# Kernel optimization log

Measured on AMD Instinct MI355X. Metric: run time of the kernel, lower is better.

The kernel has to match this reference:

```python
import jax, jax.numpy as jnp
import numpy as np

N_USERS = 100000
N_ITEMS = 50000
DIM = 64
HID = 64
E = 3200000
B = 16384


def setup_inputs() -> dict:
    key = jax.random.key(0)
    ks = jax.random.split(key, 16)
    N = N_USERS + N_ITEMS
    return {
        "users": jax.random.randint(ks[0], (B,), 0, N_USERS),
        "items": jax.random.randint(ks[1], (B,), 0, N_ITEMS),
        "edge_index": jax.random.randint(ks[2], (2, E), 0, N),
        "edge_weight": jax.random.uniform(ks[3], (E,), dtype=jnp.float32),
        # learned parameters
        "U": jax.random.normal(ks[4], (N_USERS, DIM), jnp.float32) * 0.1,
        "I": jax.random.normal(ks[5], (N_ITEMS, DIM), jnp.float32) * 0.1,
        "W0": jax.random.normal(ks[6], (DIM, HID), jnp.float32) / np.sqrt(DIM),
        "b0": jnp.zeros((HID,), jnp.float32),
        "g0": jnp.ones((HID,), jnp.float32),
        "be0": jnp.zeros((HID,), jnp.float32),
        "W1": jax.random.normal(ks[7], (HID, HID), jnp.float32) / np.sqrt(HID),
        "b1": jnp.zeros((HID,), jnp.float32),
        "g1": jnp.ones((HID,), jnp.float32),
        "be1": jnp.zeros((HID,), jnp.float32),
        "Wp": jax.random.normal(ks[8], (HID, DIM), jnp.float32) / np.sqrt(HID),
        "bp": jnp.zeros((DIM,), jnp.float32),
        "bu": jnp.zeros((N_USERS,), jnp.float32),
        "bi": jnp.zeros((N_ITEMS,), jnp.float32),
        "mu": jnp.zeros((), jnp.float32),
    }


def _layernorm(h, g, b, eps=1e-5):
    m = jnp.mean(h, axis=-1, keepdims=True)
    v = jnp.mean(jnp.square(h - m), axis=-1, keepdims=True)
    return (h - m) * jax.lax.rsqrt(v + eps) * g + b


def reference(users, items, edge_index, edge_weight, U, I,
              W0, b0, g0, be0, W1, b1, g1, be1, Wp, bp, bu, bi, mu):
    N = U.shape[0] + I.shape[0]
    x = jnp.concatenate([U, I], axis=0)  # [N, DIM]

    # GCN normalization with added self-loops (torch_geometric gcn_norm)
    loop = jnp.arange(N)
    src = jnp.concatenate([edge_index[0], loop])
    dst = jnp.concatenate([edge_index[1], loop])
    ew = jnp.concatenate([edge_weight, jnp.ones((N,), edge_weight.dtype)])
    deg = jax.ops.segment_sum(ew, dst, num_segments=N)
    dinv = jnp.where(deg > 0, jax.lax.rsqrt(deg), 0.0)
    norm = dinv[src] * ew * dinv[dst]  # [E+N]

    def conv(h, W, b):
        hw = h @ W  # [N, HID]
        msgs = norm[:, None] * hw[src]  # gather: [E+N, HID]
        return jax.ops.segment_sum(msgs, dst, num_segments=N) + b

    # layer 0: conv -> layernorm -> relu -> (dropout=identity, eval) -> residual
    h = x
    h_in = h
    h = conv(h, W0, b0)
    h = jax.nn.relu(_layernorm(h, g0, be0)) + h_in
    # layer 1
    h_in = h
    h = conv(h, W1, b1)
    h = jax.nn.relu(_layernorm(h, g1, be1)) + h_in

    h = h @ Wp + bp  # proj_out: [N, DIM]
    h_user = h[:U.shape[0]]
    h_item = h[U.shape[0]:]

    s = jnp.sum(h_user[users] * h_item[items], axis=-1)
    s = s + bu[users] + bi[items] + mu
    return jnp.clip(s, 1.0, 5.0)
```

## Files before the change

### kernel.cpp

```cpp
#include <hip/hip_runtime.h>

#define NU 100000
#define NI 50000
#define NN 150000
#define D  64
#define CAP 47
#define OVF_MAX 4096

#define BINSHIFT 8
#define BINW 256
#define NBINS 586
#define BINCAP 5848
#define STAGE_CAP 11
#define EPT 4
#define SPILL_CAP 262144
#define BIN_BLOCKS 768
#define BCPAD 16

typedef unsigned int uint;
typedef unsigned short ushort;
typedef unsigned char uchar;

__device__ __forceinline__ float half_reduce_add(float v) {
    #pragma unroll
    for (int m = 16; m >= 1; m >>= 1) v += __shfl_xor(v, m, 64);
    return v;
}
__device__ __forceinline__ ushort f2bf(float f) {
    union { float f; uint i; } c; c.f = f;
    uint r = c.i + 0x7FFF + ((c.i >> 16) & 1);
    return (ushort)(r >> 16);
}
__device__ __forceinline__ float lane_bcast(float v, int l) {
    return __int_as_float(__builtin_amdgcn_readlane(__float_as_int(v), l));
}
__device__ __forceinline__ uint enc14(float w) {
    uint b = __float_as_uint(w) + 0x00020000u;
    return b & 0xFFFC0000u;
}
__device__ __forceinline__ float dec14(uint r) {
    return __uint_as_float(r & 0xFFFC0000u);
}
__device__ __forceinline__ void spill_one(int d, uint s, float w,
        uint2* __restrict__ spill, int* __restrict__ spillcnt) {
    int si = atomicAdd(spillcnt, 1);
    if (si < SPILL_CAP) spill[si] = make_uint2(s | enc14(w), (uint)d);
}

__global__ __launch_bounds__(256) void k_bin(
        const int* __restrict__ src, const int* __restrict__ dst,
        const float* __restrict__ ew, int* __restrict__ bincur,
        uint2* __restrict__ binbuf, uint2* __restrict__ spill,
        int* __restrict__ spillcnt, uint2* __restrict__ tail,
        uchar* __restrict__ cnt8, int E) {
    __shared__ uint2 stage[NBINS][STAGE_CAP];
    __shared__ int scnt[NBINS];
    int t = threadIdx.x;
    for (int i = t; i < NBINS; i += 256) scnt[i] = 0;
    __syncthreads();
    const int batch = 256 * EPT;
    for (int base = blockIdx.x * batch; base < E; base += BIN_BLOCKS * batch) {
        int dd[EPT]; uint ss[EPT]; float ww[EPT]; int ok[EPT];
        #pragma unroll
        for (int k = 0; k < EPT; ++k) {
            int e = base + k * 256 + t;
            ok[k] = (e < E);
            if (ok[k]) { dd[k] = dst[e]; ss[k] = (uint)src[e]; ww[k] = ew[e]; }
        }
        #pragma unroll
        for (int k = 0; k < EPT; ++k) {
            if (!ok[k]) continue;
            int bin = dd[k] >> BINSHIFT;
            int slot = atomicAdd(&scnt[bin], 1);
            if (slot < STAGE_CAP) {
                stage[bin][slot] = make_uint2(
                    ss[k] | ((uint)(dd[k] & (BINW - 1)) << 18),
                    (uint)__float_as_int(ww[k]));
            } else {
                spill_one(dd[k], ss[k], ww[k], spill, spillcnt);
            }
        }
        __syncthreads();
        for (int bin = t; bin < NBINS; bin += 256) {
            int c = scnt[bin]; if (c > STAGE_CAP) c = STAGE_CAP;
            while (c >= 8) {
                int b0 = atomicAdd(&bincur[bin * BCPAD], 8);
                if (b0 + 8 <= BINCAP) {
                    uint4* o4 = (uint4*)(binbuf + (size_t)bin * BINCAP + b0);
                    uint2* s2 = &stage[bin][c - 8];
                    o4[0] = make_uint4(s2[0].x, s2[0].y, s2[1].x, s2[1].y);
                    o4[1] = make_uint4(s2[2].x, s2[2].y, s2[3].x, s2[3].y);
                    o4[2] = make_uint4(s2[4].x, s2[4].y, s2[5].x, s2[5].y);
                    o4[3] = make_uint4(s2[6].x, s2[6].y, s2[7].x, s2[7].y);
                } else {
                    for (int j = 0; j < 8; ++j) {
                        uint2 r = stage[bin][c - 8 + j];
                        spill_one((bin << BINSHIFT) + (int)(r.x >> 18),
                                  r.x & 0x3FFFFu, __int_as_float((int)r.y),
                                  spill, spillcnt);
                    }
                }
                c -= 8;
            }
            scnt[bin] = c;
        }
        __syncthreads();
    }
    uchar* cb = cnt8 + (size_t)blockIdx.x * NBINS;
    for (int i = t; i < NBINS; i += 256) cb[i] = (uchar)scnt[i];
    uint2* tb = tail + (size_t)blockIdx.x * (NBINS * 8);
    for (int i = t; i < NBINS * 8; i += 256) tb[i] = stage[i >> 3][i & 7];
}

__global__ __launch_bounds__(256) void k_regroup(
        const int* __restrict__ bincur, const uint2* __restrict__ binbuf,
        const uint2* __restrict__ spill, const int* __restrict__ spillcnt,
        const uint2* __restrict__ tail, const uchar* __restrict__ cnt8,
        uint* __restrict__ recs, int* __restrict__ cursor,
        float* __restrict__ dinv, int4* __restrict__ ovf,
        int* __restrict__ ovfcnt) {
    __shared__ uint image[256 * CAP];
    __shared__ int cnt[256];
    __shared__ float ovfw[256];
    int t = threadIdx.x;
    int bin = blockIdx.x;
    cnt[t] = 0; ovfw[t] = 0.0f;
    __syncthreads();
    int dbase = bin << BINSHIFT;
    int nrec = bincur[bin * BCPAD]; if (nrec > BINCAP) nrec = BINCAP;
    const uint2* bb = binbuf + (size_t)bin * BINCAP;
    for (int i = t; i < nrec; i += 256) {
        uint2 r = bb[i];
        int dl = (int)(r.x >> 18);
        int slot = atomicAdd(&cnt[dl], 1);
        uint s = r.x & 0x3FFFFu;
        float w = __int_as_float((int)r.y);
        if (slot < CAP) image[dl * CAP + slot] = enc14(w) | s;
        else {
            atomicAdd(&ovfw[dl], w);
            int o = atomicAdd(ovfcnt, 1);
            if (o < OVF_MAX)
                ovf[o] = make_int4(dbase + dl, (int)s, __float_as_int(w), 0);
        }
    }
    for (int g = t; g < BIN_BLOCKS; g += 256) {
        int c = cnt8[(size_t)g * NBINS + bin];
        const uint2* tb = tail + ((size_t)g * NBINS + bin) * 8;
        for (int j = 0; j < c; ++j) {
            uint2 r = tb[j];
            int dl = (int)(r.x >> 18);
            int slot = atomicAdd(&cnt[dl], 1);
            uint s = r.x & 0x3FFFFu;
            float w = __int_as_float((int)r.y);
            if (slot < CAP) image[dl * CAP + slot] = enc14(w) | s;
            else {
                atomicAdd(&ovfw[dl], w);
                int o = atomicAdd(ovfcnt, 1);
                if (o < OVF_MAX)
                    ovf[o] = make_int4(dbase + dl, (int)s, __float_as_int(w), 0);
            }
        }
    }
    int ns = spillcnt[0]; if (ns > SPILL_CAP) ns = SPILL_CAP;
    for (int i = t; i < ns; i += 256) {
        uint2 e = spill[i];
        int d = (int)e.y;
        if (d < dbase || d >= dbase + BINW) continue;
        int dl = d - dbase;
        int slot = atomicAdd(&cnt[dl], 1);
        if (slot < CAP) image[dl * CAP + slot] = e.x;
        else {
            float w = dec14(e.x);
            atomicAdd(&ovfw[dl], w);
            int o = atomicAdd(ovfcnt, 1);
            if (o < OVF_MAX) ovf[o] = make_int4(d, (int)(e.x & 0x3FFFFu),
                                                __float_as_int(w), 0);
        }
    }
    __syncthreads();
    int ndl = NN - dbase; if (ndl > 256) ndl = 256;
    if (ndl <= 0) return;
    if (t < ndl) {
        int c = cnt[t];
        cursor[dbase + t] = c;
        if (c > CAP) c = CAP;
        float dg = ovfw[t];
        for (int j = 0; j < c; ++j) dg += dec14(image[t * CAP + j]);
        dinv[dbase + t] = rsqrtf(dg + 1.0f);
    }
    int tot = ndl * CAP;
    uint* out = recs + (size_t)dbase * CAP;
    for (int i = t; i < tot; i += 256) out[i] = image[i];
}

__global__ __launch_bounds__(256) void k_gemm1(
        const float* __restrict__ U, const float* __restrict__ I,
        const float* __restrict__ W, const float* __restrict__ dinv,
        ushort* __restrict__ out) {
    int lane = threadIdx.x & 63;
    float wreg[64];
    #pragma unroll
    for (int k = 0; k < 64; ++k) wreg[k] = W[k * 64 + lane];
    int wpb = blockDim.x >> 6;
    int wid = blockIdx.x * wpb + (threadIdx.x >> 6);
    int tw = gridDim.x * wpb;
    for (int n = wid; n < NN; n += tw) {
        float xv = (n < NU) ? U[(size_t)n * D + lane]
                            : I[(size_t)(n - NU) * D + lane];
        float a0 = 0.f, a1 = 0.f, a2 = 0.f, a3 = 0.f;
        #pragma unroll
        for (int k = 0; k < 64; k += 4) {
            a0 = fmaf(lane_bcast(xv, k + 0), wreg[k + 0], a0);
            a1 = fmaf(lane_bcast(xv, k + 1), wreg[k + 1], a1);
            a2 = fmaf(lane_bcast(xv, k + 2), wreg[k + 2], a2);
            a3 = fmaf(lane_bcast(xv, k + 3), wreg[k + 3], a3);
        }
        out[(size_t)n * D + lane] = f2bf(((a0 + a1) + (a2 + a3)) * dinv[n]);
    }
}

#define CA_DECL(c) uint x##c##0, x##c##1, x##c##2, x##c##3, \
                        w##c##0, w##c##1, w##c##2, w##c##3;
#define CA_GET(c, i, P, rvv) { \
    uint r = (uint)__builtin_amdgcn_ds_bpermute(vodd4 + 8 * (P), (int)(rvv)); \
    w##c##i = r & 0xFFFC0000u; \
    x##c##i = *(const uint*)((const char*)hw2p + \
                             (((r & 0x3FFFFu) << 7) + lb4)); }
#define CA_ISSUE(c, P0, rvv) { CA_GET(c, 0, (P0)+0, rvv) CA_GET(c, 1, (P0)+1, rvv) \
                               CA_GET(c, 2, (P0)+2, rvv) CA_GET(c, 3, (P0)+3, rvv) }
#define CA_FMA1(c, i, axv, ayv) { \
    axv = fmaf(__uint_as_float(w##c##i), __uint_as_float(x##c##i << 16), axv); \
    ayv = fmaf(__uint_as_float(w##c##i), \
               __uint_as_float(x##c##i & 0xFFFF0000u), ayv); }
#define CA_FMA(c, axv, ayv) { CA_FMA1(c,0,axv,ayv) CA_FMA1(c,1,axv,ayv) \
                              CA_FMA1(c,2,axv,ayv) CA_FMA1(c,3,axv,ayv) }

__device__ __forceinline__ float2 conv_accum2(int n, int lane,
        const uint* __restrict__ hw2p, const int* __restrict__ cursor,
        const uint* __restrict__ recs, const int4* __restrict__ ovf,
        const int* __restrict__ ovfcnt) {
    int cnt = __builtin_amdgcn_readfirstlane(cursor[n]);
    if (cnt > CAP) cnt = CAP;
    uint rv = (lane < cnt) ? recs[(size_t)n * CAP + lane] : 0u;
    const int  vodd4 = (lane >> 5) << 2;
    const uint lb4   = (uint)(lane & 31) << 2;
    uint xs = *(const uint*)((const char*)hw2p + (((uint)n << 7) + lb4));
    float ax = 0.f, ay = 0.f;
    int cp = (cnt + 7) & ~7;
    CA_DECL(A) CA_DECL(B) CA_DECL(G)
    CA_ISSUE(A, 0, rv) CA_ISSUE(B, 4, rv) CA_ISSUE(G, 8, rv)
    CA_FMA(A, ax, ay)
    if (cp > 24) CA_ISSUE(A, 12, rv)
    CA_FMA(B, ax, ay)
    if (cp > 32) CA_ISSUE(B, 16, rv)
    CA_FMA(G, ax, ay)
    if (cp > 40) CA_ISSUE(G, 20, rv)
    if (cp > 24) CA_FMA(A, ax, ay)
    if (cp > 32) CA_FMA(B, ax, ay)
    if (cp > 40) CA_FMA(G, ax, ay)
    ax += __shfl_xor(ax, 32, 64);
    ay += __shfl_xor(ay, 32, 64);
    ax += __uint_as_float(xs << 16);
    ay += __uint_as_float(xs & 0xFFFF0000u);
    int novf = __builtin_amdgcn_readfirstlane(ovfcnt[0]);
    if (novf > 0) {
        if (novf > OVF_MAX) novf = OVF_MAX;
        for (int j = 0; j < novf; ++j) {
            int4 e = ovf[j];
            if (e.x == n) {
                float w = __int_as_float(e.z);
                uint x = hw2p[(size_t)e.y * 32 + (lane & 31)];
                ax = fmaf(w, __int_as_float((int)(x << 16)), ax);
                ay = fmaf(w, __int_as_float((int)(x & 0xFFFF0000u)), ay);
            }
        }
    }
    return make_float2(ax, ay);
}

__device__ __forceinline__ float2 ln_relu2(float2 a, float di, int p,
        const float* __restrict__ b, const float* __restrict__ g,
        const float* __restrict__ be) {
    float2 bb = ((const float2*)b)[p];
    float v0 = fmaf(a.x, di, bb.x);
    float v1 = fmaf(a.y, di, bb.y);
    float m = half_reduce_add(v0 + v1) * (1.0f / 64.0f);
    float d0 = v0 - m, d1 = v1 - m;
    float var = half_reduce_add(d0 * d0 + d1 * d1) * (1.0f / 64.0f);
    float rs = rsqrtf(var + 1e-5f);
    float2 gg = ((const float2*)g)[p];
    float2 ee = ((const float2*)be)[p];
    return make_float2(fmaxf(fmaf(d0 * rs, gg.x, ee.x), 0.0f),
                       fmaxf(fmaf(d1 * rs, gg.y, ee.y), 0.0f));
}

__global__ __launch_bounds__(256) void k_conv1(
        const uint* __restrict__ hw2p, const int* __restrict__ cursor,
        const uint* __restrict__ recs, const int4* __restrict__ ovf,
        const int* __restrict__ ovfcnt, const float* __restrict__ dinv,
        const float* __restrict__ b, const float* __restrict__ g,
        const float* __restrict__ be, const float* __restrict__ U,
        const float* __restrict__ I, uint* __restrict__ out1) {
    int lane = threadIdx.x & 63;
    int n = __builtin_amdgcn_readfirstlane(blockIdx.x * 4 + (threadIdx.x >> 6));
    if (n >= NN) return;
    float2 a = conv_accum2(n, lane, hw2p, cursor, recs, ovf, ovfcnt);
    int p = lane & 31;
    float2 y = ln_relu2(a, dinv[n], p, b, g, be);
    const float* R = (n < NU) ? (U + (size_t)n * D) : (I + (size_t)(n - NU) * D);
    float2 rr = ((const float2*)R)[p];
    if (lane < 32) {
        out1[(size_t)n * 32 + p] =
            (uint)f2bf(y.x + rr.x) | ((uint)f2bf(y.y + rr.y) << 16);
    }
}

#define CB_DECL(p, c) uint p##x##c##0, p##x##c##1, p##x##c##2, p##x##c##3, \
                           p##w##c##0, p##w##c##1, p##w##c##2, p##w##c##3;
#define CB_GET(p, c, i, P, rvv) { \
    uint r = (uint)__builtin_amdgcn_ds_bpermute(vodd4 + 8 * (P), (int)(rvv)); \
    p##w##c##i = r & 0xFFFC0000u; \
    p##x##c##i = *(const uint*)((const char*)hw2p + \
                                (((r & 0x3FFFFu) << 7) + lb4)); }
#define CB_ISSUE(p, c, P0, rvv) { CB_GET(p,c,0,(P0)+0,rvv) CB_GET(p,c,1,(P0)+1,rvv) \
                                  CB_GET(p,c,2,(P0)+2,rvv) CB_GET(p,c,3,(P0)+3,rvv) }
#define CB_FMA1(p, c, i, axv, ayv) { \
    axv = fmaf(__uint_as_float(p##w##c##i), \
               __uint_as_float(p##x##c##i << 16), axv); \
    ayv = fmaf(__uint_as_float(p##w##c##i), \
               __uint_as_float(p##x##c##i & 0xFFFF0000u), ayv); }
#define CB_FMA(p, c, axv, ayv) { CB_FMA1(p,c,0,axv,ayv) CB_FMA1(p,c,1,axv,ayv) \
                                 CB_FMA1(p,c,2,axv,ayv) CB_FMA1(p,c,3,axv,ayv) }

__device__ __forceinline__ void conv_accum2_dual(int nu, int ni, int lane,
        const uint* __restrict__ hw2p, const int* __restrict__ cursor,
        const uint* __restrict__ recs, const int4* __restrict__ ovf,
        const int* __restrict__ ovfcnt, float2* outu, float2* outi) {
    int cu = __builtin_amdgcn_readfirstlane(cursor[nu]); if (cu > CAP) cu = CAP;
    int ci = __builtin_amdgcn_readfirstlane(cursor[ni]); if (ci > CAP) ci = CAP;
    uint rvu = (lane < cu) ? recs[(size_t)nu * CAP + lane] : 0u;
    uint rvi = (lane < ci) ? recs[(size_t)ni * CAP + lane] : 0u;
    const int  vodd4 = (lane >> 5) << 2;
    const uint lb4   = (uint)(lane & 31) << 2;
    uint xsu = *(const uint*)((const char*)hw2p + (((uint)nu << 7) + lb4));
    uint xsi = *(const uint*)((const char*)hw2p + (((uint)ni << 7) + lb4));
    float uax = 0.f, uay = 0.f, iax = 0.f, iay = 0.f;
    int cpu_ = (cu + 7) & ~7, cpi_ = (ci + 7) & ~7;
    CB_DECL(u, A) CB_DECL(u, B) CB_DECL(u, G)
    CB_DECL(i, A) CB_DECL(i, B) CB_DECL(i, G)
    CB_ISSUE(u, A, 0, rvu) CB_ISSUE(i, A, 0, rvi)
    CB_ISSUE(u, B, 4, rvu) CB_ISSUE(i, B, 4, rvi)
    CB_ISSUE(u, G, 8, rvu) CB_ISSUE(i, G, 8, rvi)
    CB_FMA(u, A, uax, uay) CB_FMA(i, A, iax, iay)
    if (cpu_ > 24) CB_ISSUE(u, A, 12, rvu)
    if (cpi_ > 24) CB_ISSUE(i, A, 12, rvi)
    CB_FMA(u, B, uax, uay) CB_FMA(i, B, iax, iay)
    if (cpu_ > 32) CB_ISSUE(u, B, 16, rvu)
    if (cpi_ > 32) CB_ISSUE(i, B, 16, rvi)
    CB_FMA(u, G, uax, uay) CB_FMA(i, G, iax, iay)
    if (cpu_ > 40) CB_ISSUE(u, G, 20, rvu)
    if (cpi_ > 40) CB_ISSUE(i, G, 20, rvi)
    if (cpu_ > 24) CB_FMA(u, A, uax, uay)
    if (cpi_ > 24) CB_FMA(i, A, iax, iay)
    if (cpu_ > 32) CB_FMA(u, B, uax, uay)
    if (cpi_ > 32) CB_FMA(i, B, iax, iay)
    if (cpu_ > 40) CB_FMA(u, G, uax, uay)
    if (cpi_ > 40) CB_FMA(i, G, iax, iay)
    uax += __shfl_xor(uax, 32, 64); uay += __shfl_xor(uay, 32, 64);
    iax += __shfl_xor(iax, 32, 64); iay += __shfl_xor(iay, 32, 64);
    uax += __uint_as_float(xsu << 16); uay += __uint_as_float(xsu & 0xFFFF0000u);
    iax += __uint_as_float(xsi << 16); iay += __uint_as_float(xsi & 0xFFFF0000u);
    int novf = __builtin_amdgcn_readfirstlane(ovfcnt[0]);
    if (novf > 0) {
        if (novf > OVF_MAX) novf = OVF_MAX;
        for (int j = 0; j < novf; ++j) {
            int4 e = ovf[j];
            if (e.x == nu || e.x == ni) {
                float w = __int_as_float(e.z);
                uint x = hw2p[(size_t)e.y * 32 + (lane & 31)];
                float fx = __uint_as_float(x << 16);
                float fy = __uint_as_float(x & 0xFFFF0000u);
                if (e.x == nu) { uax = fmaf(w, fx, uax); uay = fmaf(w, fy, uay); }
                else           { iax = fmaf(w, fx, iax); iay = fmaf(w, fy, iay); }
            }
        }
    }
    *outu = make_float2(uax, uay);
    *outi = make_float2(iax, iay);
}

__global__ __launch_bounds__(256) void k_gemm2(
        const ushort* __restrict__ hb, const float* __restrict__ W,
        const float* __restrict__ dinv, ushort* __restrict__ out) {
    int lane = threadIdx.x & 63;
    float wreg[64];
    #pragma unroll
    for (int k = 0; k < 64; ++k) wreg[k] = W[k * 64 + lane];
    int wpb = blockDim.x >> 6;
    int wid = blockIdx.x * wpb + (threadIdx.x >> 6);
    int tw = gridDim.x * wpb;
    for (int n = wid; n < NN; n += tw) {
        float xv = __uint_as_float((uint)hb[(size_t)n * D + lane] << 16);
        float a0 = 0.f, a1 = 0.f, a2 = 0.f, a3 = 0.f;
        #pragma unroll
        for (int k = 0; k < 64; k += 4) {
            a0 = fmaf(lane_bcast(xv, k + 0), wreg[k + 0], a0);
            a1 = fmaf(lane_bcast(xv, k + 1), wreg[k + 1], a1);
            a2 = fmaf(lane_bcast(xv, k + 2), wreg[k + 2], a2);
            a3 = fmaf(lane_bcast(xv, k + 3), wreg[k + 3], a3);
        }
        out[(size_t)n * D + lane] = f2bf(((a0 + a1) + (a2 + a3)) * dinv[n]);
    }
}

__global__ __launch_bounds__(256) void k_conv2score(
        const uint* __restrict__ hw2p, const int* __restrict__ cursor,
        const uint* __restrict__ recs, const int4* __restrict__ ovf,
        const int* __restrict__ ovfcnt, const float* __restrict__ dinv,
        const float* __restrict__ b, const float* __restrict__ g,
        const float* __restrict__ be, const int* __restrict__ users,
        const int* __restrict__ items, const uint* __restrict__ h1b,
        const float* __restrict__ Wp, const float* __restrict__ bp,
        const float* __restrict__ bu, const float* __restrict__ bi,
        const float* __restrict__ mu, float* __restrict__ out, int B) {
    __shared__ float wlds[64 * 64];
    int t = threadIdx.x;
    for (int i = t; i < 64 * 64; i += 256) wlds[i] = Wp[i];
    __syncthreads();
    int lane = t & 63;
    float bpl = bp[lane];
    int q = lane & 31;
    int wpb = blockDim.x >> 6;
    int wid = blockIdx.x * wpb + (t >> 6);
    int tw = gridDim.x * wpb;
    for (int p = wid; p < B; p += tw) {
        int un = users[p];
        int in_ = NU + items[p];
        int nu = __builtin_amdgcn_readfirstlane(un);
        int ni = __builtin_amdgcn_readfirstlane(in_);
        float2 au, ai;
        conv_accum2_dual(nu, ni, lane, hw2p, cursor, recs, ovf, ovfcnt,
                         &au, &ai);
        float2 yu = ln_relu2(au, dinv[nu], q, b, g, be);
        float2 yi = ln_relu2(ai, dinv[ni], q, b, g, be);
        uint xu = h1b[(size_t)nu * 32 + q];
        uint xi = h1b[(size_t)ni * 32 + q];
        float2 hu = make_float2(yu.x + __uint_as_float(xu << 16),
                                yu.y + __uint_as_float(xu & 0xFFFF0000u));
        float2 hi = make_float2(yi.x + __uint_as_float(xi << 16),
                                yi.y + __uint_as_float(xi & 0xFFFF0000u));
        float pu = bpl, pi = bpl;
        #pragma unroll
        for (int j = 0; j < 32; ++j) {
            float w0 = wlds[(2 * j) * 64 + lane];
            float w1 = wlds[(2 * j + 1) * 64 + lane];
            pu = fmaf(lane_bcast(hu.x, j), w0, pu);
            pu = fmaf(lane_bcast(hu.y, j), w1, pu);
            pi = fmaf(lane_bcast(hi.x, j), w0, pi);
            pi = fmaf(lane_bcast(hi.y, j), w1, pi);
        }
        float dot = pu * pi;
        #pragma unroll
        for (int m = 32; m >= 1; m >>= 1) dot += __shfl_xor(dot, m, 64);
        if (lane == 0) {
            dot += bu[un] + bi[in_ - NU] + mu[0];
            out[p] = fminf(fmaxf(dot, 1.0f), 5.0f);
        }
    }
}

extern "C" void kernel_launch(void* const* d_in, const int* in_sizes, int n_in,
                              void* d_out, int out_size, void* d_ws, size_t ws_size,
                              hipStream_t stream) {
    const int*   users = (const int*)d_in[0];
    const int*   items = (const int*)d_in[1];
    const int*   ei2   = (const int*)d_in[2];
    const float* ew    = (const float*)d_in[3];
    const float* U     = (const float*)d_in[4];
    const float* I     = (const float*)d_in[5];
    const float* W0    = (const float*)d_in[6];
    const float* b0    = (const float*)d_in[7];
    const float* g0    = (const float*)d_in[8];
    const float* be0   = (const float*)d_in[9];
    const float* W1    = (const float*)d_in[10];
    const float* b1    = (const float*)d_in[11];
    const float* g1    = (const float*)d_in[12];
    const float* be1   = (const float*)d_in[13];
    const float* Wp    = (const float*)d_in[14];
    const float* bp    = (const float*)d_in[15];
    const float* bu    = (const float*)d_in[16];
    const float* bi    = (const float*)d_in[17];
    const float* mu    = (const float*)d_in[18];

    int B = in_sizes[0];
    int E = in_sizes[2] / 2;
    const int* srcp = ei2;
    const int* dstp = ei2 + E;

    char* p = (char*)d_ws;
    auto alloc = [&](size_t bytes) -> char* {
        char* r = p;
        p += (bytes + 255) & ~(size_t)255;
        return r;
    };
    int*    cbuf    = (int*)  alloc((size_t)(NBINS * BCPAD + 32) * 4);
    int*    bincur  = cbuf;
    int*    spillcnt= cbuf + NBINS * BCPAD;
    int*    ovfcnt  = cbuf + NBINS * BCPAD + 16;
    int*    cursor  = (int*)  alloc((size_t)NN * 4);
    float*  dinv    = (float*)alloc((size_t)NN * 4);
    int4*   ovf     = (int4*) alloc((size_t)OVF_MAX * 16);
    uint2*  spill   = (uint2*)alloc((size_t)SPILL_CAP * 8);
    uchar*  cnt8    = (uchar*)alloc((size_t)BIN_BLOCKS * NBINS);
    uint2*  binbuf  = (uint2*)alloc((size_t)NBINS * BINCAP * 8);
    uint*   recs    = (uint*) alloc((size_t)NN * CAP * 4);
    ushort* hw2b    = (ushort*)alloc((size_t)NN * D * 2);
    uint*   h1b     = (uint*) alloc((size_t)NN * 32 * 4);
    const uint* hw2p = (const uint*)hw2b;
    uint2*  tail    = (uint2*)hw2b;

    hipMemsetAsync(cbuf, 0, (size_t)(NBINS * BCPAD + 32) * 4, stream);

    int gW = (NN + 3) / 4;

    k_bin<<<BIN_BLOCKS, 256, 0, stream>>>(srcp, dstp, ew, bincur, binbuf,
                                          spill, spillcnt, tail, cnt8, E);
    k_regroup<<<NBINS, 256, 0, stream>>>(bincur, binbuf, spill, spillcnt,
                                         tail, cnt8, recs, cursor, dinv,
                                         ovf, ovfcnt);

    k_gemm1<<<2048, 256, 0, stream>>>(U, I, W0, dinv, hw2b);
    k_conv1<<<gW, 256, 0, stream>>>(hw2p, cursor, recs, ovf, ovfcnt, dinv,
                                    b0, g0, be0, U, I, h1b);
    k_gemm2<<<2048, 256, 0, stream>>>((const ushort*)h1b, W1, dinv, hw2b);
    k_conv2score<<<2048, 256, 0, stream>>>(hw2p, cursor, recs, ovf, ovfcnt, dinv,
                                           b1, g1, be1, users, items, h1b,
                                           Wp, bp, bu, bi, mu,
                                           (float*)d_out, B);
}
```

Before: 403.7 us.

## Fuse first GEMM into regroup, drop global spill list, shrink per-block tails

The layer-0 feature transform (x @ W0 scaled by dinv) moves into the regroup kernel, where each bin block computes it for its own 256 nodes using dinv values already held in shared memory. This removes a separate kernel launch and a global dinv reread. The global spill list is replaced by direct single-record atomic appends into the per-bin buffer, so the regroup kernel no longer scans the whole spill array once per bin. Per-block tails shrink from 8 to 5 entries with the excess flushed to binbuf, EPT is raised to 8, and the tail buffer moves to h1b because hw2b is now written during regroup.

```diff
diff --git a/kernel.cpp b/kernel.cpp
--- a/kernel.cpp
+++ b/kernel.cpp
@@ -12,10 +12,10 @@
 #define NBINS 586
 #define BINCAP 5848
 #define STAGE_CAP 11
-#define EPT 4
-#define SPILL_CAP 262144
+#define EPT 8
 #define BIN_BLOCKS 768
 #define BCPAD 16
+#define TAILS 5
 
 typedef unsigned int uint;
 typedef unsigned short ushort;
@@ -41,17 +41,11 @@
 __device__ __forceinline__ float dec14(uint r) {
     return __uint_as_float(r & 0xFFFC0000u);
 }
-__device__ __forceinline__ void spill_one(int d, uint s, float w,
-        uint2* __restrict__ spill, int* __restrict__ spillcnt) {
-    int si = atomicAdd(spillcnt, 1);
-    if (si < SPILL_CAP) spill[si] = make_uint2(s | enc14(w), (uint)d);
-}
 
 __global__ __launch_bounds__(256) void k_bin(
         const int* __restrict__ src, const int* __restrict__ dst,
         const float* __restrict__ ew, int* __restrict__ bincur,
-        uint2* __restrict__ binbuf, uint2* __restrict__ spill,
-        int* __restrict__ spillcnt, uint2* __restrict__ tail,
+        uint2* __restrict__ binbuf, uint2* __restrict__ tail,
         uchar* __restrict__ cnt8, int E) {
     __shared__ uint2 stage[NBINS][STAGE_CAP];
     __shared__ int scnt[NBINS];
@@ -71,13 +65,15 @@
         for (int k = 0; k < EPT; ++k) {
             if (!ok[k]) continue;
             int bin = dd[k] >> BINSHIFT;
+            uint2 rec = make_uint2(
+                ss[k] | ((uint)(dd[k] & (BINW - 1)) << 18),
+                (uint)__float_as_int(ww[k]));
             int slot = atomicAdd(&scnt[bin], 1);
             if (slot < STAGE_CAP) {
-                stage[bin][slot] = make_uint2(
-                    ss[k] | ((uint)(dd[k] & (BINW - 1)) << 18),
-                    (uint)__float_as_int(ww[k]));
+                stage[bin][slot] = rec;
             } else {
-                spill_one(dd[k], ss[k], ww[k], spill, spillcnt);
+                int b0 = atomicAdd(&bincur[bin * BCPAD], 1);
+                if (b0 < BINCAP) binbuf[(size_t)bin * BINCAP + b0] = rec;
             }
         }
         __syncthreads();
@@ -92,13 +88,6 @@
                     o4[1] = make_uint4(s2[2].x, s2[2].y, s2[3].x, s2[3].y);
                     o4[2] = make_uint4(s2[4].x, s2[4].y, s2[5].x, s2[5].y);
                     o4[3] = make_uint4(s2[6].x, s2[6].y, s2[7].x, s2[7].y);
-                } else {
-                    for (int j = 0; j < 8; ++j) {
-                        uint2 r = stage[bin][c - 8 + j];
-                        spill_one((bin << BINSHIFT) + (int)(r.x >> 18),
-                                  r.x & 0x3FFFFu, __int_as_float((int)r.y),
-                                  spill, spillcnt);
-                    }
                 }
                 c -= 8;
             }
@@ -107,18 +96,31 @@
         __syncthreads();
     }
     uchar* cb = cnt8 + (size_t)blockIdx.x * NBINS;
-    for (int i = t; i < NBINS; i += 256) cb[i] = (uchar)scnt[i];
-    uint2* tb = tail + (size_t)blockIdx.x * (NBINS * 8);
-    for (int i = t; i < NBINS * 8; i += 256) tb[i] = stage[i >> 3][i & 7];
+    for (int bin = t; bin < NBINS; bin += 256) {
+        int c = scnt[bin]; if (c > STAGE_CAP) c = STAGE_CAP;
+        if (c > TAILS) {
+            for (int j = TAILS; j < c; ++j) {
+                int b0 = atomicAdd(&bincur[bin * BCPAD], 1);
+                if (b0 < BINCAP) binbuf[(size_t)bin * BINCAP + b0] =
+                    stage[bin][j];
+            }
+            c = TAILS;
+        }
+        cb[bin] = (uchar)c;
+    }
+    uint2* tb = tail + (size_t)blockIdx.x * (NBINS * TAILS);
+    for (int i = t; i < NBINS * TAILS; i += 256)
+        tb[i] = stage[i / TAILS][i % TAILS];
 }
 
 __global__ __launch_bounds__(256) void k_regroup(
         const int* __restrict__ bincur, const uint2* __restrict__ binbuf,
-        const uint2* __restrict__ spill, const int* __restrict__ spillcnt,
         const uint2* __restrict__ tail, const uchar* __restrict__ cnt8,
         uint* __restrict__ recs, int* __restrict__ cursor,
         float* __restrict__ dinv, int4* __restrict__ ovf,
-        int* __restrict__ ovfcnt) {
+        int* __restrict__ ovfcnt,
+        const float* __restrict__ U, const float* __restrict__ I,
+        const float* __restrict__ W0, ushort* __restrict__ hw2b) {
     __shared__ uint image[256 * CAP];
     __shared__ int cnt[256];
     __shared__ float ovfw[256];
@@ -145,7 +147,7 @@
     }
     for (int g = t; g < BIN_BLOCKS; g += 256) {
         int c = cnt8[(size_t)g * NBINS + bin];
-        const uint2* tb = tail + ((size_t)g * NBINS + bin) * 8;
+        const uint2* tb = tail + ((size_t)g * NBINS + bin) * TAILS;
         for (int j = 0; j < c; ++j) {
             uint2 r = tb[j];
             int dl = (int)(r.x >> 18);
@@ -161,22 +163,6 @@
             }
         }
     }
-    int ns = spillcnt[0]; if (ns > SPILL_CAP) ns = SPILL_CAP;
-    for (int i = t; i < ns; i += 256) {
-        uint2 e = spill[i];
-        int d = (int)e.y;
-        if (d < dbase || d >= dbase + BINW) continue;
-        int dl = d - dbase;
-        int slot = atomicAdd(&cnt[dl], 1);
-        if (slot < CAP) image[dl * CAP + slot] = e.x;
-        else {
-            float w = dec14(e.x);
-            atomicAdd(&ovfw[dl], w);
-            int o = atomicAdd(ovfcnt, 1);
-            if (o < OVF_MAX) ovf[o] = make_int4(d, (int)(e.x & 0x3FFFFu),
-                                                __float_as_int(w), 0);
-        }
-    }
     __syncthreads();
     int ndl = NN - dbase; if (ndl > 256) ndl = 256;
     if (ndl <= 0) return;
@@ -186,36 +172,35 @@
         if (c > CAP) c = CAP;
         float dg = ovfw[t];
         for (int j = 0; j < c; ++j) dg += dec14(image[t * CAP + j]);
-        dinv[dbase + t] = rsqrtf(dg + 1.0f);
+        float dv = rsqrtf(dg + 1.0f);
+        dinv[dbase + t] = dv;
+        ovfw[t] = dv;
     }
     int tot = ndl * CAP;
     uint* out = recs + (size_t)dbase * CAP;
     for (int i = t; i < tot; i += 256) out[i] = image[i];
-}
-
-__global__ __launch_bounds__(256) void k_gemm1(
-        const float* __restrict__ U, const float* __restrict__ I,
-        const float* __restrict__ W, const float* __restrict__ dinv,
-        ushort* __restrict__ out) {
-    int lane = threadIdx.x & 63;
-    float wreg[64];
-    #pragma unroll
-    for (int k = 0; k < 64; ++k) wreg[k] = W[k * 64 + lane];
-    int wpb = blockDim.x >> 6;
-    int wid = blockIdx.x * wpb + (threadIdx.x >> 6);
-    int tw = gridDim.x * wpb;
-    for (int n = wid; n < NN; n += tw) {
-        float xv = (n < NU) ? U[(size_t)n * D + lane]
-                            : I[(size_t)(n - NU) * D + lane];
-        float a0 = 0.f, a1 = 0.f, a2 = 0.f, a3 = 0.f;
+    __syncthreads();
+    {
+        int lane = t & 63;
+        int wv = t >> 6;
+        float wreg[64];
         #pragma unroll
-        for (int k = 0; k < 64; k += 4) {
-            a0 = fmaf(lane_bcast(xv, k + 0), wreg[k + 0], a0);
-            a1 = fmaf(lane_bcast(xv, k + 1), wreg[k + 1], a1);
-            a2 = fmaf(lane_bcast(xv, k + 2), wreg[k + 2], a2);
-            a3 = fmaf(lane_bcast(xv, k + 3), wreg[k + 3], a3);
-        }
-        out[(size_t)n * D + lane] = f2bf(((a0 + a1) + (a2 + a3)) * dinv[n]);
+        for (int k = 0; k < 64; ++k) wreg[k] = W0[k * 64 + lane];
+        for (int j = wv; j < ndl; j += 4) {
+            int n = dbase + j;
+            float xv = (n < NU) ? U[(size_t)n * D + lane]
+                                : I[(size_t)(n - NU) * D + lane];
+            float a0 = 0.f, a1 = 0.f, a2 = 0.f, a3 = 0.f;
+            #pragma unroll
+            for (int k = 0; k < 64; k += 4) {
+                a0 = fmaf(lane_bcast(xv, k + 0), wreg[k + 0], a0);
+                a1 = fmaf(lane_bcast(xv, k + 1), wreg[k + 1], a1);
+                a2 = fmaf(lane_bcast(xv, k + 2), wreg[k + 2], a2);
+                a3 = fmaf(lane_bcast(xv, k + 3), wreg[k + 3], a3);
+            }
+            hw2b[(size_t)n * D + lane] =
+                f2bf(((a0 + a1) + (a2 + a3)) * ovfw[j]);
+        }
     }
 }
 
@@ -505,31 +490,28 @@
     };
     int*    cbuf    = (int*)  alloc((size_t)(NBINS * BCPAD + 32) * 4);
     int*    bincur  = cbuf;
-    int*    spillcnt= cbuf + NBINS * BCPAD;
     int*    ovfcnt  = cbuf + NBINS * BCPAD + 16;
     int*    cursor  = (int*)  alloc((size_t)NN * 4);
     float*  dinv    = (float*)alloc((size_t)NN * 4);
     int4*   ovf     = (int4*) alloc((size_t)OVF_MAX * 16);
-    uint2*  spill   = (uint2*)alloc((size_t)SPILL_CAP * 8);
     uchar*  cnt8    = (uchar*)alloc((size_t)BIN_BLOCKS * NBINS);
     uint2*  binbuf  = (uint2*)alloc((size_t)NBINS * BINCAP * 8);
     uint*   recs    = (uint*) alloc((size_t)NN * CAP * 4);
     ushort* hw2b    = (ushort*)alloc((size_t)NN * D * 2);
     uint*   h1b     = (uint*) alloc((size_t)NN * 32 * 4);
     const uint* hw2p = (const uint*)hw2b;
-    uint2*  tail    = (uint2*)hw2b;
+    uint2*  tail    = (uint2*)h1b;
 
     hipMemsetAsync(cbuf, 0, (size_t)(NBINS * BCPAD + 32) * 4, stream);
 
     int gW = (NN + 3) / 4;
 
     k_bin<<<BIN_BLOCKS, 256, 0, stream>>>(srcp, dstp, ew, bincur, binbuf,
-                                          spill, spillcnt, tail, cnt8, E);
-    k_regroup<<<NBINS, 256, 0, stream>>>(bincur, binbuf, spill, spillcnt,
-                                         tail, cnt8, recs, cursor, dinv,
-                                         ovf, ovfcnt);
-
-    k_gemm1<<<2048, 256, 0, stream>>>(U, I, W0, dinv, hw2b);
+                                          tail, cnt8, E);
+    k_regroup<<<NBINS, 256, 0, stream>>>(bincur, binbuf, tail, cnt8,
+                                         recs, cursor, dinv, ovf, ovfcnt,
+                                         U, I, W0, hw2b);
+
     k_conv1<<<gW, 256, 0, stream>>>(hw2p, cursor, recs, ovf, ovfcnt, dinv,
                                     b0, g0, be0, U, I, h1b);
     k_gemm2<<<2048, 256, 0, stream>>>((const ushort*)h1b, W1, dinv, hw2b);
```

Measured after the change: 403.2 us. Within noise of the previous version (-0.1%).
